# Performance work log

Hardware: AMD Instinct MI355X
Metric: run time of the kernel (lower is better)

The kernel has to match this reference:

```python
import jax, jax.numpy as jnp
import numpy as np

N_SENTS, N_ENTS, BATCH, DIM, HEADS = 64, 16, 64, 512, 8


def setup_inputs() -> dict:
    key = jax.random.key(0)
    ks = jax.random.split(key, 10)
    se = N_SENTS * N_ENTS
    s = 0.02  # init scale for projection weights
    entities = jax.random.normal(ks[0], (se, BATCH, DIM), dtype=jnp.float32)
    query_param = jax.random.uniform(ks[1], (1, 1, DIM), jnp.float32, -1.0, 1.0)
    wq = jax.random.normal(ks[2], (DIM, DIM), jnp.float32) * s
    wk = jax.random.normal(ks[3], (DIM, DIM), jnp.float32) * s
    wv = jax.random.normal(ks[4], (DIM, DIM), jnp.float32) * s
    wo = jax.random.normal(ks[5], (DIM, DIM), jnp.float32) * s
    bq = jax.random.normal(ks[6], (DIM,), jnp.float32) * s
    bk = jax.random.normal(ks[7], (DIM,), jnp.float32) * s
    bv = jax.random.normal(ks[8], (DIM,), jnp.float32) * s
    bo = jax.random.normal(ks[9], (DIM,), jnp.float32) * s
    return {"entities": entities, "query_param": query_param,
            "wq": wq, "wk": wk, "wv": wv, "wo": wo,
            "bq": bq, "bk": bk, "bv": bv, "bo": bo,
            "n_sents": N_SENTS}


def reference(entities, query_param, wq, wk, wv, wo, bq, bk, bv, bo, n_sents):
    # entities: [n_sents*n_ents, batch, dim]
    se, b, d = entities.shape
    n_ents = se // n_sents
    h = HEADS
    hd = d // h

    # Learned single query broadcast to every (sentence, batch) slot.
    q_in = jnp.broadcast_to(query_param, (n_sents, b, d))
    q = q_in @ wq.T + bq            # [n_sents, b, d]
    k = entities @ wk.T + bk        # [se, b, d]
    v = entities @ wv.T + bv        # [se, b, d]

    # Split heads -> [b, h, len, hd]
    qh = q.reshape(n_sents, b, h, hd).transpose(1, 2, 0, 3)
    kh = k.reshape(se, b, h, hd).transpose(1, 2, 0, 3)
    vh = v.reshape(se, b, h, hd).transpose(1, 2, 0, 3)

    scale = jnp.asarray(1.0 / np.sqrt(hd), dtype=qh.dtype)
    scores = jnp.einsum('bhqd,bhkd->bhqk', qh, kh) * scale  # [b,h,n_sents,se]

    # Block-diagonal mask: query i attends only to keys [i*n_ents, (i+1)*n_ents)
    valid = (jnp.arange(se) // n_ents)[None, :] == jnp.arange(n_sents)[:, None]
    scores = jnp.where(valid[None, None], scores, jnp.finfo(scores.dtype).min)

    attn = jax.nn.softmax(scores, axis=-1)
    ctx = jnp.einsum('bhqk,bhkd->bhqd', attn, vh)            # [b,h,n_sents,hd]
    out = ctx.transpose(2, 0, 1, 3).reshape(n_sents, b, d)   # merge heads
    return out @ wo.T + bo                                   # [n_sents, b, d]
```

## Files before the change

kernel.cpp:

```cpp
#include <hip/hip_runtime.h>
#include <stdint.h>

#define HEADS 8
#define DIM   512
#define HD    64
#define NE    16
#define NS    64
#define NB    64

typedef short bf16x8 __attribute__((ext_vector_type(8)));
typedef float f32x4  __attribute__((ext_vector_type(4)));

__device__ __forceinline__ unsigned short f2bf(float f) {
    union { float f; uint32_t u; } v; v.f = f;
    uint32_t u = v.u;
    u += 0x7fffu + ((u >> 16) & 1u);
    return (unsigned short)(u >> 16);
}
__device__ __forceinline__ float bf2f(unsigned short b) {
    union { uint32_t u; float f; } v; v.u = ((uint32_t)b) << 16;
    return v.f;
}

__global__ __launch_bounds__(256) void k_prep(
    const float* __restrict__ qp, const float* __restrict__ wq,
    const float* __restrict__ bq, const float* __restrict__ wv,
    const float* __restrict__ wo, float* __restrict__ qvec,
    unsigned short* __restrict__ wv_bf, unsigned short* __restrict__ wo_bf)
{
    const int bid = blockIdx.x;
    const int t = threadIdx.x;
    if (bid < 64) {
        const int dl = t >> 5, js = t & 31;
        const int d = bid * 8 + dl;
        const float* w = wq + (size_t)d * DIM + js * 16;
        const float* q = qp + js * 16;
        float acc = 0.f;
        #pragma unroll
        for (int i = 0; i < 16; i++) acc += w[i] * q[i];
        #pragma unroll
        for (int msk = 16; msk >= 1; msk >>= 1) acc += __shfl_xor(acc, msk);
        if (js == 0) qvec[d] = acc + bq[d];
        return;
    }
    const bool is_v = bid < 320;
    const float* src = is_v ? wv : wo;
    unsigned short* dst = is_v ? wv_bf : wo_bf;
    const int li = ((is_v ? bid - 64 : bid - 320) * 1024 + t * 4);
    const float4 v = *(const float4*)(src + li);
    ushort4 hv;
    hv.x = f2bf(v.x); hv.y = f2bf(v.y); hv.z = f2bf(v.z); hv.w = f2bf(v.w);
    *(ushort4*)(dst + li) = hv;
}

__global__ __launch_bounds__(64) void k_uproj(
    const float* __restrict__ qvec, const float* __restrict__ wk,
    unsigned short* __restrict__ u_bf)
{
    const int bid = blockIdx.x;
    const int l = threadIdx.x;
    if (bid >= 64) {
        const int row = 8 + (bid - 64);
        ((uint4*)(u_bf + row * DIM))[l & 63] = (uint4){0u, 0u, 0u, 0u};
        return;
    }
    const int h = bid >> 3, cg = bid & 7;
    __shared__ float qs[HD];
    qs[l] = qvec[h * HD + l];
    __syncthreads();
    const int c = cg * 64 + l;
    const float* w = wk + (size_t)(h * HD) * DIM + c;
    float acc = 0.f;
    #pragma unroll 8
    for (int j = 0; j < HD; j++) acc += qs[j] * w[(size_t)j * DIM];
    u_bf[h * DIM + c] = f2bf(acc);
}

__global__ __launch_bounds__(256, 2) void k_attn(
    const float* __restrict__ ents, const unsigned short* __restrict__ u_bf,
    unsigned short* __restrict__ weighted)
{
    __shared__ unsigned short ent[NE * 4 * DIM];
    __shared__ float attn_s[4][NE][16];
    const int t = threadIdx.x;
    const int bid = blockIdx.x;
    const int s = bid >> 4;
    const int bg = (bid & 15) << 2;

    {
        const float* base = ents + ((size_t)(s * NE) * NB + bg) * DIM;
        #pragma unroll 4
        for (int i = 0; i < 32; i++) {
            const int li = t + 256 * i;
            const int e  = li >> 9;
            const int bb = (li >> 7) & 3;
            const int d0 = (li & 127) << 2;
            const float4 v = *(const float4*)(base + ((size_t)e * NB + bb) * DIM + d0);
            ushort4 hv;
            hv.x = f2bf(v.x); hv.y = f2bf(v.y); hv.z = f2bf(v.z); hv.w = f2bf(v.w);
            const uint32_t off = (uint32_t)((((e * 4 + bb) << 9) + d0) << 1) ^ (uint32_t)((e & 7) << 4);
            *(ushort4*)((char*)ent + off) = hv;
        }
    }
    __syncthreads();

    const int w = t >> 6, l = t & 63;
    const int m = l & 15, g = l >> 4;

    {
        const uint32_t aswz = (uint32_t)((m & 7) << 4);
        const uint32_t abase = (uint32_t)((m * 4 + w) << 10);
        const unsigned short* urow = u_bf + m * DIM;
        f32x4 acc = {0.f, 0.f, 0.f, 0.f};
        #pragma unroll
        for (int kk = 0; kk < DIM; kk += 32) {
            const int kp = kk + g * 8;
            bf16x8 af = *(const bf16x8*)((const char*)ent + ((abase + (uint32_t)(kp << 1)) ^ aswz));
            bf16x8 bf = *(const bf16x8*)(urow + kp);
            acc = __builtin_amdgcn_mfma_f32_16x16x32_bf16(af, bf, acc, 0, 0, 0);
        }
        const float scale = 0.125f;
        float s0 = acc[0]*scale, s1 = acc[1]*scale, s2 = acc[2]*scale, s3 = acc[3]*scale;
        float mx = fmaxf(fmaxf(s0, s1), fmaxf(s2, s3));
        mx = fmaxf(mx, __shfl_xor(mx, 16));
        mx = fmaxf(mx, __shfl_xor(mx, 32));
        const float p0 = __expf(s0 - mx), p1 = __expf(s1 - mx);
        const float p2 = __expf(s2 - mx), p3 = __expf(s3 - mx);
        float sm = p0 + p1 + p2 + p3;
        sm += __shfl_xor(sm, 16);
        sm += __shfl_xor(sm, 32);
        const float inv = 1.f / sm;
        attn_s[w][4 * g + 0][m] = p0 * inv;
        attn_s[w][4 * g + 1][m] = p1 * inv;
        attn_s[w][4 * g + 2][m] = p2 * inv;
        attn_s[w][4 * g + 3][m] = p3 * inv;
    }
    __syncthreads();

    float acc2[HEADS][8];
    #pragma unroll
    for (int h = 0; h < HEADS; h++)
        #pragma unroll
        for (int j = 0; j < 8; j++) acc2[h][j] = 0.f;

    const int d0 = l << 3;
    #pragma unroll
    for (int e = 0; e < NE; e++) {
        const uint32_t off = (uint32_t)((((e * 4 + w) << 9) + d0) << 1) ^ (uint32_t)((e & 7) << 4);
        const bf16x8 ev = *(const bf16x8*)((const char*)ent + off);
        const unsigned short* ep = (const unsigned short*)&ev;
        float evf[8];
        #pragma unroll
        for (int j = 0; j < 8; j++) evf[j] = bf2f(ep[j]);
        const float4 a0 = *(const float4*)&attn_s[w][e][0];
        const float4 a1 = *(const float4*)&attn_s[w][e][4];
        float av[8] = {a0.x, a0.y, a0.z, a0.w, a1.x, a1.y, a1.z, a1.w};
        #pragma unroll
        for (int h = 0; h < HEADS; h++)
            #pragma unroll
            for (int j = 0; j < 8; j++) acc2[h][j] += av[h] * evf[j];
    }
    unsigned short* wrow = weighted + ((size_t)(s * NB + bg + w) << 12);
    #pragma unroll
    for (int h = 0; h < HEADS; h++) {
        bf16x8 ov;
        #pragma unroll
        for (int j = 0; j < 8; j++) ov[j] = (short)f2bf(acc2[h][j]);
        *(bf16x8*)(wrow + h * DIM + d0) = ov;
    }
}

template <typename CT>
__global__ __launch_bounds__(256) void k_gemm(
    const unsigned short* __restrict__ A, int lda, int aOffY,
    const unsigned short* __restrict__ B, int ldb, int bOffY,
    const float* __restrict__ bias, CT* __restrict__ C, int ldc, int cOffY, int K)
{
    __shared__ unsigned short a_s[64][72];
    __shared__ unsigned short b_s[64][72];
    const int t = threadIdx.x;
    const int m0 = blockIdx.x * 64;
    const int y  = blockIdx.y;
    const int w = t >> 6, l = t & 63;
    const int m = l & 15, g = l >> 4;
    const int lr = t >> 2, lk = (t & 3) * 16;

    const unsigned short* Ap = A + (size_t)(m0 + lr) * lda + (size_t)aOffY * y;
    const unsigned short* Bp = B + (size_t)(bOffY * y + lr) * ldb;

    f32x4 acc[4];
    #pragma unroll
    for (int i = 0; i < 4; i++) acc[i] = (f32x4){0.f, 0.f, 0.f, 0.f};

    for (int k0 = 0; k0 < K; k0 += 64) {
        const ushort4 av0 = *(const ushort4*)(Ap + k0 + lk);
        const ushort4 av1 = *(const ushort4*)(Ap + k0 + lk + 4);
        const ushort4 av2 = *(const ushort4*)(Ap + k0 + lk + 8);
        const ushort4 av3 = *(const ushort4*)(Ap + k0 + lk + 12);
        const ushort4 bv0 = *(const ushort4*)(Bp + k0 + lk);
        const ushort4 bv1 = *(const ushort4*)(Bp + k0 + lk + 4);
        const ushort4 bv2 = *(const ushort4*)(Bp + k0 + lk + 8);
        const ushort4 bv3 = *(const ushort4*)(Bp + k0 + lk + 12);
        *(ushort4*)&a_s[lr][lk]      = av0;
        *(ushort4*)&a_s[lr][lk + 4]  = av1;
        *(ushort4*)&a_s[lr][lk + 8]  = av2;
        *(ushort4*)&a_s[lr][lk + 12] = av3;
        *(ushort4*)&b_s[lr][lk]      = bv0;
        *(ushort4*)&b_s[lr][lk + 4]  = bv1;
        *(ushort4*)&b_s[lr][lk + 8]  = bv2;
        *(ushort4*)&b_s[lr][lk + 12] = bv3;
        __syncthreads();
        #pragma unroll
        for (int kk = 0; kk < 64; kk += 32) {
            const int kp = kk + g * 8;
            const bf16x8 af = *(const bf16x8*)&a_s[w * 16 + m][kp];
            const bf16x8 b0 = *(const bf16x8*)&b_s[ 0 + m][kp];
            const bf16x8 b1 = *(const bf16x8*)&b_s[16 + m][kp];
            const bf16x8 b2 = *(const bf16x8*)&b_s[32 + m][kp];
            const bf16x8 b3 = *(const bf16x8*)&b_s[48 + m][kp];
            acc[0] = __builtin_amdgcn_mfma_f32_16x16x32_bf16(af, b0, acc[0], 0, 0, 0);
            acc[1] = __builtin_amdgcn_mfma_f32_16x16x32_bf16(af, b1, acc[1], 0, 0, 0);
            acc[2] = __builtin_amdgcn_mfma_f32_16x16x32_bf16(af, b2, acc[2], 0, 0, 0);
            acc[3] = __builtin_amdgcn_mfma_f32_16x16x32_bf16(af, b3, acc[3], 0, 0, 0);
        }
        __syncthreads();
    }

    const int colbase = cOffY * y;
    #pragma unroll
    for (int nt = 0; nt < 4; nt++) {
        const int col = colbase + nt * 16 + m;
        const float bs = bias[col];
        #pragma unroll
        for (int j = 0; j < 4; j++) {
            const int row = m0 + w * 16 + g * 4 + j;
            const float val = acc[nt][j] + bs;
            if (sizeof(CT) == 2) {
                ((unsigned short*)C)[(size_t)row * ldc + col] = f2bf(val);
            } else {
                ((float*)C)[(size_t)row * ldc + col] = val;
            }
        }
    }
}

extern "C" void kernel_launch(void* const* d_in, const int* in_sizes, int n_in,
                              void* d_out, int out_size, void* d_ws, size_t ws_size,
                              hipStream_t stream)
{
    const float* ents = (const float*)d_in[0];
    const float* qp   = (const float*)d_in[1];
    const float* wq   = (const float*)d_in[2];
    const float* wk   = (const float*)d_in[3];
    const float* wv   = (const float*)d_in[4];
    const float* wo   = (const float*)d_in[5];
    const float* bq   = (const float*)d_in[6];
    const float* bv   = (const float*)d_in[8];
    const float* bo   = (const float*)d_in[9];

    char* ws = (char*)d_ws;
    float*          qvec     = (float*)ws;
    unsigned short* u_bf     = (unsigned short*)(ws + 4096);
    unsigned short* wv_bf    = (unsigned short*)(ws + 65536);
    unsigned short* wo_bf    = (unsigned short*)(ws + 65536 + 524288);
    unsigned short* weighted = (unsigned short*)(ws + 2097152);
    unsigned short* ctx      = (unsigned short*)(ws + 2097152 + 33554432);

    k_prep <<<576, 256, 0, stream>>>(qp, wq, bq, wv, wo, qvec, wv_bf, wo_bf);
    k_uproj<<<72, 64, 0, stream>>>(qvec, wk, u_bf);
    k_attn <<<1024, 256, 0, stream>>>(ents, u_bf, weighted);
    k_gemm<unsigned short><<<dim3(64, 8), 256, 0, stream>>>(
        weighted, HEADS * DIM, DIM, wv_bf, DIM, HD, bv, ctx, DIM, HD, DIM);
    k_gemm<float><<<dim3(64, 8), 256, 0, stream>>>(
        ctx, DIM, 0, wo_bf, DIM, HD, bo, (float*)d_out, DIM, HD, DIM);
}
```

Baseline: 68.30 us.

## Pipeline attention with double-buffered async global-to-LDS loads in fp32

Rewrites the attention kernel as a persistent-style loop: each of 256 blocks processes 8 tiles of 2 batch rows, using global_load_lds DMA to double-buffer the fp32 entity tiles in LDS while computing the current tile. The bf16 conversion of entities and the MFMA score computation are dropped in favour of fp32 VALU dot products against an fp32 u matrix held in LDS, with swizzled layouts to avoid bank conflicts. Softmax moves to a small shared-memory reduction per tile. The aim is to hide HBM latency behind compute, at the cost of one block per CU, extra barriers per tile, and more VALU work.

```diff
diff --git a/kernel.cpp b/kernel.cpp
--- a/kernel.cpp
+++ b/kernel.cpp
@@ -17,9 +17,10 @@
     u += 0x7fffu + ((u >> 16) & 1u);
     return (unsigned short)(u >> 16);
 }
-__device__ __forceinline__ float bf2f(unsigned short b) {
-    union { uint32_t u; float f; } v; v.u = ((uint32_t)b) << 16;
-    return v.f;
+
+__device__ __forceinline__ void bar_lds() {
+    asm volatile("s_waitcnt lgkmcnt(0)" ::: "memory");
+    __builtin_amdgcn_s_barrier();
 }
 
 __global__ __launch_bounds__(256) void k_prep(
@@ -55,16 +56,10 @@
 
 __global__ __launch_bounds__(64) void k_uproj(
     const float* __restrict__ qvec, const float* __restrict__ wk,
-    unsigned short* __restrict__ u_bf)
-{
-    const int bid = blockIdx.x;
+    float* __restrict__ u_f)
+{
+    const int h = blockIdx.x >> 3, cg = blockIdx.x & 7;
     const int l = threadIdx.x;
-    if (bid >= 64) {
-        const int row = 8 + (bid - 64);
-        ((uint4*)(u_bf + row * DIM))[l & 63] = (uint4){0u, 0u, 0u, 0u};
-        return;
-    }
-    const int h = bid >> 3, cg = bid & 7;
     __shared__ float qs[HD];
     qs[l] = qvec[h * HD + l];
     __syncthreads();
@@ -73,100 +68,135 @@
     float acc = 0.f;
     #pragma unroll 8
     for (int j = 0; j < HD; j++) acc += qs[j] * w[(size_t)j * DIM];
-    u_bf[h * DIM + c] = f2bf(acc);
-}
-
-__global__ __launch_bounds__(256, 2) void k_attn(
-    const float* __restrict__ ents, const unsigned short* __restrict__ u_bf,
+    u_f[h * DIM + c] = acc;
+}
+
+__device__ __forceinline__ void issue_tile_dma(
+    const float* __restrict__ ents, float* lds_buf, int tau, int w, int lane)
+{
+    const int s = tau >> 5, bg = (tau & 31) << 1;
+    #pragma unroll
+    for (int i = 0; i < 16; i++) {
+        const int p  = ((w * 16 + i) << 6) | lane;
+        const int e  = p >> 8;
+        const int bb = (p >> 7) & 1;
+        const int jp = p & 127;
+        const int j  = jp ^ (e & 7);
+        const float* src = ents + ((((size_t)(s * NE + e)) * NB + (bg + bb)) << 9) + (j << 2);
+        float* dst = lds_buf + ((w * 16 + i) << 8);
+        __builtin_amdgcn_global_load_lds(
+            (const __attribute__((address_space(1))) void*)src,
+            (__attribute__((address_space(3))) void*)dst, 16, 0, 0);
+    }
+}
+
+__global__ __launch_bounds__(256, 1) void k_attn(
+    const float* __restrict__ ents, const float* __restrict__ u_f,
     unsigned short* __restrict__ weighted)
 {
-    __shared__ unsigned short ent[NE * 4 * DIM];
-    __shared__ float attn_s[4][NE][16];
+    __shared__ float ent_s[2][16384];
+    __shared__ float u_s[4096];
+    __shared__ float score_s[256];
+    __shared__ float attn_s[256];
+    __shared__ float m_s[16], inv_s[16];
+
     const int t = threadIdx.x;
-    const int bid = blockIdx.x;
-    const int s = bid >> 4;
-    const int bg = (bid & 15) << 2;
-
-    {
-        const float* base = ents + ((size_t)(s * NE) * NB + bg) * DIM;
-        #pragma unroll 4
-        for (int i = 0; i < 32; i++) {
-            const int li = t + 256 * i;
-            const int e  = li >> 9;
-            const int bb = (li >> 7) & 3;
-            const int d0 = (li & 127) << 2;
-            const float4 v = *(const float4*)(base + ((size_t)e * NB + bb) * DIM + d0);
-            ushort4 hv;
-            hv.x = f2bf(v.x); hv.y = f2bf(v.y); hv.z = f2bf(v.z); hv.w = f2bf(v.w);
-            const uint32_t off = (uint32_t)((((e * 4 + bb) << 9) + d0) << 1) ^ (uint32_t)((e & 7) << 4);
-            *(ushort4*)((char*)ent + off) = hv;
-        }
+    const int w = t >> 6, lane = t & 63;
+
+    #pragma unroll
+    for (int r = 0; r < 4; r++) {
+        const int g = t + 256 * r;
+        const int h = g >> 7, j = g & 127;
+        const int ju = j ^ ((j >> 4) & 7);
+        const f32x4 v = *(const f32x4*)(u_f + g * 4);
+        *(f32x4*)&u_s[((h << 7) | ju) << 2] = v;
     }
     __syncthreads();
 
-    const int w = t >> 6, l = t & 63;
-    const int m = l & 15, g = l >> 4;
-
-    {
-        const uint32_t aswz = (uint32_t)((m & 7) << 4);
-        const uint32_t abase = (uint32_t)((m * 4 + w) << 10);
-        const unsigned short* urow = u_bf + m * DIM;
-        f32x4 acc = {0.f, 0.f, 0.f, 0.f};
-        #pragma unroll
-        for (int kk = 0; kk < DIM; kk += 32) {
-            const int kp = kk + g * 8;
-            bf16x8 af = *(const bf16x8*)((const char*)ent + ((abase + (uint32_t)(kp << 1)) ^ aswz));
-            bf16x8 bf = *(const bf16x8*)(urow + kp);
-            acc = __builtin_amdgcn_mfma_f32_16x16x32_bf16(af, bf, acc, 0, 0, 0);
-        }
-        const float scale = 0.125f;
-        float s0 = acc[0]*scale, s1 = acc[1]*scale, s2 = acc[2]*scale, s3 = acc[3]*scale;
-        float mx = fmaxf(fmaxf(s0, s1), fmaxf(s2, s3));
-        mx = fmaxf(mx, __shfl_xor(mx, 16));
-        mx = fmaxf(mx, __shfl_xor(mx, 32));
-        const float p0 = __expf(s0 - mx), p1 = __expf(s1 - mx);
-        const float p2 = __expf(s2 - mx), p3 = __expf(s3 - mx);
-        float sm = p0 + p1 + p2 + p3;
-        sm += __shfl_xor(sm, 16);
-        sm += __shfl_xor(sm, 32);
-        const float inv = 1.f / sm;
-        attn_s[w][4 * g + 0][m] = p0 * inv;
-        attn_s[w][4 * g + 1][m] = p1 * inv;
-        attn_s[w][4 * g + 2][m] = p2 * inv;
-        attn_s[w][4 * g + 3][m] = p3 * inv;
-    }
-    __syncthreads();
-
-    float acc2[HEADS][8];
-    #pragma unroll
-    for (int h = 0; h < HEADS; h++)
-        #pragma unroll
-        for (int j = 0; j < 8; j++) acc2[h][j] = 0.f;
-
-    const int d0 = l << 3;
-    #pragma unroll
-    for (int e = 0; e < NE; e++) {
-        const uint32_t off = (uint32_t)((((e * 4 + w) << 9) + d0) << 1) ^ (uint32_t)((e & 7) << 4);
-        const bf16x8 ev = *(const bf16x8*)((const char*)ent + off);
-        const unsigned short* ep = (const unsigned short*)&ev;
-        float evf[8];
-        #pragma unroll
-        for (int j = 0; j < 8; j++) evf[j] = bf2f(ep[j]);
-        const float4 a0 = *(const float4*)&attn_s[w][e][0];
-        const float4 a1 = *(const float4*)&attn_s[w][e][4];
-        float av[8] = {a0.x, a0.y, a0.z, a0.w, a1.x, a1.y, a1.z, a1.w};
-        #pragma unroll
-        for (int h = 0; h < HEADS; h++)
+    const int tau0 = blockIdx.x * 8;
+    issue_tile_dma(ents, ent_s[0], tau0, w, lane);
+    asm volatile("s_waitcnt vmcnt(0)" ::: "memory");
+    __builtin_amdgcn_s_barrier();
+
+    const int bb = t >> 7;
+    const int e  = (t >> 3) & 15;
+    const int dp = t & 7;
+    const int dc = t & 127;
+    const int ebase = ((e << 1) | bb) << 7;
+    const int esw = e & 7;
+
+    for (int it = 0; it < 8; ++it) {
+        const int tau = tau0 + it;
+        const int cur = it & 1;
+        const float* buf = ent_s[cur];
+
+        if (it < 7) issue_tile_dma(ents, ent_s[cur ^ 1], tau + 1, w, lane);
+
+        float pt[8] = {0.f, 0.f, 0.f, 0.f, 0.f, 0.f, 0.f, 0.f};
+        #pragma unroll
+        for (int jj = 0; jj < 16; jj++) {
+            const int jg = (dp << 4) | jj;
+            const f32x4 ev = *(const f32x4*)&buf[(ebase | (jg ^ esw)) << 2];
             #pragma unroll
-            for (int j = 0; j < 8; j++) acc2[h][j] += av[h] * evf[j];
-    }
-    unsigned short* wrow = weighted + ((size_t)(s * NB + bg + w) << 12);
-    #pragma unroll
-    for (int h = 0; h < HEADS; h++) {
-        bf16x8 ov;
-        #pragma unroll
-        for (int j = 0; j < 8; j++) ov[j] = (short)f2bf(acc2[h][j]);
-        *(bf16x8*)(wrow + h * DIM + d0) = ov;
+            for (int h = 0; h < 8; h++) {
+                const f32x4 uv = *(const f32x4*)&u_s[((h << 7) | (jg ^ dp)) << 2];
+                pt[h] += ev.x * uv.x + ev.y * uv.y + ev.z * uv.z + ev.w * uv.w;
+            }
+        }
+        #pragma unroll
+        for (int msk = 1; msk <= 4; msk <<= 1)
+            #pragma unroll
+            for (int h = 0; h < 8; h++) pt[h] += __shfl_xor(pt[h], msk);
+        float sc = pt[0];
+        #pragma unroll
+        for (int h = 1; h < 8; h++) sc = (dp == h) ? pt[h] : sc;
+        sc *= 0.125f;
+        score_s[t] = sc;
+        bar_lds();
+
+        if (t < 16) {
+            const int lb = t >> 3, lh = t & 7;
+            float mx = -1e30f;
+            #pragma unroll
+            for (int ee = 0; ee < 16; ee++)
+                mx = fmaxf(mx, score_s[(((lb << 4) | ee) << 3) | lh]);
+            float sum = 0.f;
+            #pragma unroll
+            for (int ee = 0; ee < 16; ee++)
+                sum += __expf(score_s[(((lb << 4) | ee) << 3) | lh] - mx);
+            m_s[t] = mx; inv_s[t] = 1.f / sum;
+        }
+        bar_lds();
+
+        attn_s[t] = __expf(sc - m_s[(bb << 3) | dp]) * inv_s[(bb << 3) | dp];
+        bar_lds();
+
+        f32x4 acc0 = {0,0,0,0}, acc1 = {0,0,0,0}, acc2 = {0,0,0,0}, acc3 = {0,0,0,0};
+        f32x4 acc4 = {0,0,0,0}, acc5 = {0,0,0,0}, acc6 = {0,0,0,0}, acc7 = {0,0,0,0};
+        #pragma unroll
+        for (int ee = 0; ee < 16; ee++) {
+            const f32x4 ev = *(const f32x4*)&buf[((((ee << 1) | bb) << 7) | (dc ^ (ee & 7))) << 2];
+            const f32x4 a0 = *(const f32x4*)&attn_s[((bb << 4) | ee) << 3];
+            const f32x4 a1 = *(const f32x4*)&attn_s[(((bb << 4) | ee) << 3) + 4];
+            acc0 += a0.x * ev; acc1 += a0.y * ev; acc2 += a0.z * ev; acc3 += a0.w * ev;
+            acc4 += a1.x * ev; acc5 += a1.y * ev; acc6 += a1.z * ev; acc7 += a1.w * ev;
+        }
+        {
+            const int s = tau >> 5, bg = (tau & 31) << 1;
+            unsigned short* wrow = weighted + ((size_t)(s * NB + bg + bb) << 12) + (dc << 2);
+            ushort4 o;
+            o.x=f2bf(acc0.x); o.y=f2bf(acc0.y); o.z=f2bf(acc0.z); o.w=f2bf(acc0.w); *(ushort4*)(wrow + 0*DIM) = o;
+            o.x=f2bf(acc1.x); o.y=f2bf(acc1.y); o.z=f2bf(acc1.z); o.w=f2bf(acc1.w); *(ushort4*)(wrow + 1*DIM) = o;
+            o.x=f2bf(acc2.x); o.y=f2bf(acc2.y); o.z=f2bf(acc2.z); o.w=f2bf(acc2.w); *(ushort4*)(wrow + 2*DIM) = o;
+            o.x=f2bf(acc3.x); o.y=f2bf(acc3.y); o.z=f2bf(acc3.z); o.w=f2bf(acc3.w); *(ushort4*)(wrow + 3*DIM) = o;
+            o.x=f2bf(acc4.x); o.y=f2bf(acc4.y); o.z=f2bf(acc4.z); o.w=f2bf(acc4.w); *(ushort4*)(wrow + 4*DIM) = o;
+            o.x=f2bf(acc5.x); o.y=f2bf(acc5.y); o.z=f2bf(acc5.z); o.w=f2bf(acc5.w); *(ushort4*)(wrow + 5*DIM) = o;
+            o.x=f2bf(acc6.x); o.y=f2bf(acc6.y); o.z=f2bf(acc6.z); o.w=f2bf(acc6.w); *(ushort4*)(wrow + 6*DIM) = o;
+            o.x=f2bf(acc7.x); o.y=f2bf(acc7.y); o.z=f2bf(acc7.z); o.w=f2bf(acc7.w); *(ushort4*)(wrow + 7*DIM) = o;
+        }
+
+        if (it < 7) asm volatile("s_waitcnt vmcnt(8)" ::: "memory");
+        __builtin_amdgcn_s_barrier();
     }
 }
 
@@ -260,15 +290,15 @@
 
     char* ws = (char*)d_ws;
     float*          qvec     = (float*)ws;
-    unsigned short* u_bf     = (unsigned short*)(ws + 4096);
+    float*          u_f      = (float*)(ws + 4096);
     unsigned short* wv_bf    = (unsigned short*)(ws + 65536);
     unsigned short* wo_bf    = (unsigned short*)(ws + 65536 + 524288);
     unsigned short* weighted = (unsigned short*)(ws + 2097152);
     unsigned short* ctx      = (unsigned short*)(ws + 2097152 + 33554432);
 
     k_prep <<<576, 256, 0, stream>>>(qp, wq, bq, wv, wo, qvec, wv_bf, wo_bf);
-    k_uproj<<<72, 64, 0, stream>>>(qvec, wk, u_bf);
-    k_attn <<<1024, 256, 0, stream>>>(ents, u_bf, weighted);
+    k_uproj<<<64, 64, 0, stream>>>(qvec, wk, u_f);
+    k_attn <<<256, 256, 0, stream>>>(ents, u_f, weighted);
     k_gemm<unsigned short><<<dim3(64, 8), 256, 0, stream>>>(
         weighted, HEADS * DIM, DIM, wv_bf, DIM, HD, bv, ctx, DIM, HD, DIM);
     k_gemm<float><<<dim3(64, 8), 256, 0, stream>>>(
```

Measured after the change: 93.37 us. 1.37x slower.

## Drop LDS staging in attention kernel, read entities directly from global per wave

Applied to the files above, without the earlier changes.

The attention kernel no longer stages a bf16 copy of the entity tile in shared memory. Each wave now reads fp32 entities straight from global memory for both the score MFMA and the weighted sum. This removes the large LDS buffer and both block barriers, which should raise occupancy, and the weighted sum now runs in fp32 on the original values. The cost is that entities are read from global memory twice (relying on cache hits), and the change also adds packed bf16 conversion instructions, a block-index swizzle, and a regrouping of the uproj launch.

```diff
diff --git a/kernel.cpp b/kernel.cpp
--- a/kernel.cpp
+++ b/kernel.cpp
@@ -17,9 +17,14 @@
     u += 0x7fffu + ((u >> 16) & 1u);
     return (unsigned short)(u >> 16);
 }
-__device__ __forceinline__ float bf2f(unsigned short b) {
-    union { uint32_t u; float f; } v; v.u = ((uint32_t)b) << 16;
-    return v.f;
+
+__device__ __forceinline__ bf16x8 cvt8(float4 lo, float4 hi) {
+    union { uint32_t u[4]; bf16x8 v; } r;
+    asm("v_cvt_pk_bf16_f32 %0, %1, %2" : "=v"(r.u[0]) : "v"(lo.x), "v"(lo.y));
+    asm("v_cvt_pk_bf16_f32 %0, %1, %2" : "=v"(r.u[1]) : "v"(lo.z), "v"(lo.w));
+    asm("v_cvt_pk_bf16_f32 %0, %1, %2" : "=v"(r.u[2]) : "v"(hi.x), "v"(hi.y));
+    asm("v_cvt_pk_bf16_f32 %0, %1, %2" : "=v"(r.u[3]) : "v"(hi.z), "v"(hi.w));
+    return r.v;
 }
 
 __global__ __launch_bounds__(256) void k_prep(
@@ -53,22 +58,22 @@
     *(ushort4*)(dst + li) = hv;
 }
 
-__global__ __launch_bounds__(64) void k_uproj(
+__global__ __launch_bounds__(256) void k_uproj(
     const float* __restrict__ qvec, const float* __restrict__ wk,
     unsigned short* __restrict__ u_bf)
 {
     const int bid = blockIdx.x;
-    const int l = threadIdx.x;
-    if (bid >= 64) {
-        const int row = 8 + (bid - 64);
-        ((uint4*)(u_bf + row * DIM))[l & 63] = (uint4){0u, 0u, 0u, 0u};
+    const int t = threadIdx.x;
+    if (bid >= 16) {
+        const int row = 8 + (bid - 16) * 4 + (t >> 6);
+        ((uint4*)(u_bf + row * DIM))[t & 63] = (uint4){0u, 0u, 0u, 0u};
         return;
     }
-    const int h = bid >> 3, cg = bid & 7;
+    const int h = bid >> 1;
+    const int c = (bid & 1) * 256 + t;
     __shared__ float qs[HD];
-    qs[l] = qvec[h * HD + l];
+    if (t < HD) qs[t] = qvec[h * HD + t];
     __syncthreads();
-    const int c = cg * 64 + l;
     const float* w = wk + (size_t)(h * HD) * DIM + c;
     float acc = 0.f;
     #pragma unroll 8
@@ -76,49 +81,32 @@
     u_bf[h * DIM + c] = f2bf(acc);
 }
 
-__global__ __launch_bounds__(256, 2) void k_attn(
+__global__ __launch_bounds__(256) void k_attn(
     const float* __restrict__ ents, const unsigned short* __restrict__ u_bf,
     unsigned short* __restrict__ weighted)
 {
-    __shared__ unsigned short ent[NE * 4 * DIM];
-    __shared__ float attn_s[4][NE][16];
-    const int t = threadIdx.x;
-    const int bid = blockIdx.x;
+    __shared__ float attn_s[4][NE][8];
+    const int t = threadIdx.x;
+    const int w = t >> 6, lane = t & 63;
+    const int bid = ((int)blockIdx.x & 7) * 128 + ((int)blockIdx.x >> 3);
     const int s = bid >> 4;
-    const int bg = (bid & 15) << 2;
+    const int b = ((bid & 15) << 2) | w;
+
+    const int m = lane & 15, g = lane >> 4;
+
+    const float* aptr = ents + (((size_t)(s * NE + m)) * NB + b) * DIM + g * 8;
+    const unsigned short* urow = u_bf + m * DIM + g * 8;
+    f32x4 acc = {0.f, 0.f, 0.f, 0.f};
+    #pragma unroll
+    for (int ks = 0; ks < 16; ks++) {
+        const float4 f0 = *(const float4*)(aptr + ks * 32);
+        const float4 f1 = *(const float4*)(aptr + ks * 32 + 4);
+        const bf16x8 af = cvt8(f0, f1);
+        const bf16x8 bf = *(const bf16x8*)(urow + ks * 32);
+        acc = __builtin_amdgcn_mfma_f32_16x16x32_bf16(af, bf, acc, 0, 0, 0);
+    }
 
     {
-        const float* base = ents + ((size_t)(s * NE) * NB + bg) * DIM;
-        #pragma unroll 4
-        for (int i = 0; i < 32; i++) {
-            const int li = t + 256 * i;
-            const int e  = li >> 9;
-            const int bb = (li >> 7) & 3;
-            const int d0 = (li & 127) << 2;
-            const float4 v = *(const float4*)(base + ((size_t)e * NB + bb) * DIM + d0);
-            ushort4 hv;
-            hv.x = f2bf(v.x); hv.y = f2bf(v.y); hv.z = f2bf(v.z); hv.w = f2bf(v.w);
-            const uint32_t off = (uint32_t)((((e * 4 + bb) << 9) + d0) << 1) ^ (uint32_t)((e & 7) << 4);
-            *(ushort4*)((char*)ent + off) = hv;
-        }
-    }
-    __syncthreads();
-
-    const int w = t >> 6, l = t & 63;
-    const int m = l & 15, g = l >> 4;
-
-    {
-        const uint32_t aswz = (uint32_t)((m & 7) << 4);
-        const uint32_t abase = (uint32_t)((m * 4 + w) << 10);
-        const unsigned short* urow = u_bf + m * DIM;
-        f32x4 acc = {0.f, 0.f, 0.f, 0.f};
-        #pragma unroll
-        for (int kk = 0; kk < DIM; kk += 32) {
-            const int kp = kk + g * 8;
-            bf16x8 af = *(const bf16x8*)((const char*)ent + ((abase + (uint32_t)(kp << 1)) ^ aswz));
-            bf16x8 bf = *(const bf16x8*)(urow + kp);
-            acc = __builtin_amdgcn_mfma_f32_16x16x32_bf16(af, bf, acc, 0, 0, 0);
-        }
         const float scale = 0.125f;
         float s0 = acc[0]*scale, s1 = acc[1]*scale, s2 = acc[2]*scale, s3 = acc[3]*scale;
         float mx = fmaxf(fmaxf(s0, s1), fmaxf(s2, s3));
@@ -130,43 +118,42 @@
         sm += __shfl_xor(sm, 16);
         sm += __shfl_xor(sm, 32);
         const float inv = 1.f / sm;
-        attn_s[w][4 * g + 0][m] = p0 * inv;
-        attn_s[w][4 * g + 1][m] = p1 * inv;
-        attn_s[w][4 * g + 2][m] = p2 * inv;
-        attn_s[w][4 * g + 3][m] = p3 * inv;
-    }
-    __syncthreads();
-
-    float acc2[HEADS][8];
-    #pragma unroll
-    for (int h = 0; h < HEADS; h++)
-        #pragma unroll
-        for (int j = 0; j < 8; j++) acc2[h][j] = 0.f;
-
-    const int d0 = l << 3;
+        if (m < HEADS) {
+            attn_s[w][4 * g + 0][m] = p0 * inv;
+            attn_s[w][4 * g + 1][m] = p1 * inv;
+            attn_s[w][4 * g + 2][m] = p2 * inv;
+            attn_s[w][4 * g + 3][m] = p3 * inv;
+        }
+    }
+
+    const int d0 = lane << 3;
+    f32x4 accA[HEADS], accB[HEADS];
+    #pragma unroll
+    for (int h = 0; h < HEADS; h++) { accA[h] = (f32x4){0,0,0,0}; accB[h] = (f32x4){0,0,0,0}; }
+
+    const float* erow = ents + (((size_t)(s * NE)) * NB + b) * DIM + d0;
     #pragma unroll
     for (int e = 0; e < NE; e++) {
-        const uint32_t off = (uint32_t)((((e * 4 + w) << 9) + d0) << 1) ^ (uint32_t)((e & 7) << 4);
-        const bf16x8 ev = *(const bf16x8*)((const char*)ent + off);
-        const unsigned short* ep = (const unsigned short*)&ev;
-        float evf[8];
-        #pragma unroll
-        for (int j = 0; j < 8; j++) evf[j] = bf2f(ep[j]);
-        const float4 a0 = *(const float4*)&attn_s[w][e][0];
-        const float4 a1 = *(const float4*)&attn_s[w][e][4];
-        float av[8] = {a0.x, a0.y, a0.z, a0.w, a1.x, a1.y, a1.z, a1.w};
-        #pragma unroll
-        for (int h = 0; h < HEADS; h++)
-            #pragma unroll
-            for (int j = 0; j < 8; j++) acc2[h][j] += av[h] * evf[j];
-    }
-    unsigned short* wrow = weighted + ((size_t)(s * NB + bg + w) << 12);
+        const float* ep = erow + (size_t)e * (NB * DIM);
+        const f32x4 e0 = *(const f32x4*)(ep);
+        const f32x4 e1 = *(const f32x4*)(ep + 4);
+        const f32x4 a0 = *(const f32x4*)&attn_s[w][e][0];
+        const f32x4 a1 = *(const f32x4*)&attn_s[w][e][4];
+        accA[0] += a0.x * e0; accB[0] += a0.x * e1;
+        accA[1] += a0.y * e0; accB[1] += a0.y * e1;
+        accA[2] += a0.z * e0; accB[2] += a0.z * e1;
+        accA[3] += a0.w * e0; accB[3] += a0.w * e1;
+        accA[4] += a1.x * e0; accB[4] += a1.x * e1;
+        accA[5] += a1.y * e0; accB[5] += a1.y * e1;
+        accA[6] += a1.z * e0; accB[6] += a1.z * e1;
+        accA[7] += a1.w * e0; accB[7] += a1.w * e1;
+    }
+    unsigned short* wrow = weighted + ((size_t)(s * NB + b) << 12) + d0;
     #pragma unroll
     for (int h = 0; h < HEADS; h++) {
-        bf16x8 ov;
-        #pragma unroll
-        for (int j = 0; j < 8; j++) ov[j] = (short)f2bf(acc2[h][j]);
-        *(bf16x8*)(wrow + h * DIM + d0) = ov;
+        const bf16x8 ov = cvt8((float4){accA[h].x, accA[h].y, accA[h].z, accA[h].w},
+                               (float4){accB[h].x, accB[h].y, accB[h].z, accB[h].w});
+        *(bf16x8*)(wrow + h * DIM) = ov;
     }
 }
 
@@ -267,7 +254,7 @@
     unsigned short* ctx      = (unsigned short*)(ws + 2097152 + 33554432);
 
     k_prep <<<576, 256, 0, stream>>>(qp, wq, bq, wv, wo, qvec, wv_bf, wo_bf);
-    k_uproj<<<72, 64, 0, stream>>>(qvec, wk, u_bf);
+    k_uproj<<<18, 256, 0, stream>>>(qvec, wk, u_bf);
     k_attn <<<1024, 256, 0, stream>>>(ents, u_bf, weighted);
     k_gemm<unsigned short><<<dim3(64, 8), 256, 0, stream>>>(
         weighted, HEADS * DIM, DIM, wv_bf, DIM, HD, bv, ctx, DIM, HD, DIM);
```

After: 74.29 us. +8.8%, slower.
